# Kernel optimization log

Hardware: AMD Instinct MI355X
Metric: run time of the kernel (lower is better)

Reference implementation:

```python
import jax, jax.numpy as jnp
import numpy as np

B, L, D = 2, 1024, 1024
H, KV, CH = 16, 4, 8          # attn heads, kv heads, context-manager heads
HD = D // H                   # 64
E, K, FF = 8, 2, 4 * D        # experts, top-k, ffn hidden
DC = 4                        # conv kernel size
EPS = 1e-6


def setup_inputs() -> dict:
    key = jax.random.key(0)
    ks = jax.random.split(key, 32)
    s = 0.02
    n = lambda k, shp: jax.random.normal(k, shp, jnp.float32) * s
    return {
        'x': jax.random.normal(ks[0], (B, L, D), jnp.float32),
        'mask': jnp.ones((B, L), jnp.int32),
        'w_rms1': jnp.ones((D,), jnp.float32),
        'w_rms2': jnp.ones((D,), jnp.float32),
        'w_rms3': jnp.ones((D,), jnp.float32),
        'w_rms4': jnp.ones((D,), jnp.float32),
        'Wq': n(ks[1], (D, D)), 'Wk': n(ks[2], (D, KV * HD)),
        'Wv': n(ks[3], (D, KV * HD)), 'Wo': n(ks[4], (D, D)),
        'Cq': n(ks[5], (D, D)), 'Ck': n(ks[6], (D, D)),
        'Cv': n(ks[7], (D, D)), 'Co': n(ks[8], (D, D)),
        'Wi': n(ks[9], (D, 2 * D)), 'bi': jnp.zeros((2 * D,), jnp.float32),
        'conv_w': n(ks[10], (D, 1, DC)), 'conv_b': jnp.zeros((D,), jnp.float32),
        'Wod': n(ks[11], (D, D)), 'bod': jnp.zeros((D,), jnp.float32),
        'w_gate': n(ks[12], (E, D)),
        'W1': n(ks[13], (E, D, FF)), 'b1': jnp.zeros((E, FF), jnp.float32),
        'W2': n(ks[14], (E, FF, D)), 'b2': jnp.zeros((E, D), jnp.float32),
    }


def _rmsnorm(x, w):
    rms = jnp.sqrt(jnp.mean(x * x, axis=-1, keepdims=True) + EPS)
    return w * (x / rms)


def _mha(x, mask, Wq, Wk, Wv, Wo, nh, nkv):
    b, l, d = x.shape
    hd = d // nh
    q = (x @ Wq).reshape(b, l, nh, hd)
    k = (x @ Wk).reshape(b, l, nkv, hd)
    v = (x @ Wv).reshape(b, l, nkv, hd)
    if nh != nkv:
        rep = nh // nkv
        k = jnp.repeat(k, rep, axis=2)
        v = jnp.repeat(v, rep, axis=2)
    scores = jnp.einsum('bqhd,bkhd->bhqk', q, k) * (hd ** -0.5)
    scores = jnp.where(mask[:, None, None, :] == 0, -jnp.inf, scores)
    attn = jax.nn.softmax(scores, axis=-1)
    out = jnp.einsum('bhqk,bkhd->bqhd', attn, v).reshape(b, l, d)
    return out @ Wo


def _deltanet(x, Wi, bi, conv_w, conv_b, Wod, bod):
    gv = x @ Wi + bi
    gate, value = jnp.split(gv, 2, axis=-1)
    # depthwise causal conv1d (kernel DC, left pad DC-1, truncated to L)
    v_ncl = jnp.transpose(value, (0, 2, 1))  # [B, D, L]
    conv = jax.lax.conv_general_dilated(
        v_ncl, conv_w, window_strides=(1,), padding=[(DC - 1, 0)],
        feature_group_count=D, dimension_numbers=('NCH', 'OIH', 'NCH'))
    conv = conv + conv_b[None, :, None]
    conv = jnp.transpose(conv, (0, 2, 1))  # [B, L, D]
    gated = conv * jax.nn.silu(gate)
    return gated @ Wod + bod


def _moe(x, w_gate, W1, b1, W2, b2):
    b, l, d = x.shape
    flat = x.reshape(-1, d)                                  # [T, D]
    gate = jax.nn.softmax(flat @ w_gate.T, axis=-1)          # [T, E]
    topk_scores, topk_idx = jax.lax.top_k(gate, K)           # [T, K]
    onehot = jax.nn.one_hot(topk_idx, E, dtype=flat.dtype)   # [T, K, E]
    combine = jnp.sum(topk_scores[..., None] * onehot, axis=1)  # [T, E]
    h = jnp.einsum('td,edh->teh', flat, W1) + b1
    h = jax.nn.gelu(h, approximate=False)
    y = jnp.einsum('teh,ehd->ted', h, W2) + b2
    out = jnp.einsum('ted,te->td', y, combine)
    return out.reshape(b, l, d)


def reference(x, mask, w_rms1, w_rms2, w_rms3, w_rms4,
              Wq, Wk, Wv, Wo, Cq, Ck, Cv, Co,
              Wi, bi, conv_w, conv_b, Wod, bod,
              w_gate, W1, b1, W2, b2):
    # eval mode: dropout = identity. multi_token_pred output is discarded by the block.
    res1 = x
    h = _rmsnorm(x, w_rms1)
    h = res1 + _mha(h, mask, Wq, Wk, Wv, Wo, H, KV)
    res2 = h
    # ContextManager stand-in: 8-head softmax self-attention (source unavailable)
    cm = _mha(h, mask, Cq, Ck, Cv, Co, CH, CH)
    h = res2 + cm
    res3 = h
    g = _rmsnorm(h, w_rms2)
    h = res3 + _deltanet(g, Wi, bi, conv_w, conv_b, Wod, bod)
    res4 = h
    g = _rmsnorm(h, w_rms3)
    h = res4 + _moe(g, w_gate, W1, b1, W2, b2)
    h = _rmsnorm(h, w_rms4)
    return h
```

## Files before the change

### kernel.cpp

```cpp
#include <hip/hip_runtime.h>
#include <hip/hip_bf16.h>
#include <math.h>

#define T_TOK 2048
#define B_SZ 2
#define L_SEQ 1024
#define D_MOD 1024
#define N_H 16
#define N_KV 4
#define N_CH 8
#define N_E 8
#define FF_DIM 4096
#define DC_K 4
#define EPS_F 1e-6f

typedef unsigned short u16;
typedef unsigned int u32;
typedef short s16x8 __attribute__((ext_vector_type(8)));
typedef u16 u16x8 __attribute__((ext_vector_type(8)));
typedef float f32x4 __attribute__((ext_vector_type(4)));
struct alignas(8) U16x4 { u16 a, b, c, d; };

__device__ __forceinline__ float gelu_exact(float x) {
    return 0.5f * x * (1.0f + erff(x * 0.70710678118654752f));
}
__device__ __forceinline__ u16 f2bf(float f) {
    u32 x = __float_as_uint(f);
    return (u16)((x + 0x7fffu + ((x >> 16) & 1u)) >> 16);
}
__device__ __forceinline__ float b2f(u16 u) {
    return __uint_as_float(((u32)u) << 16);
}
__device__ __forceinline__ void gload_lds16(const u16* g, u16* l) {
    __builtin_amdgcn_global_load_lds(
        (const __attribute__((address_space(1))) u32*)g,
        (__attribute__((address_space(3))) u32*)l, 16, 0, 0);
}
__device__ __forceinline__ int swz(int row, int ch, int cpr) {
    return (cpr == 4) ? (ch ^ ((row >> 1) & 3)) : (ch ^ (row & 7));
}

struct TDesc {
    const float* src;
    u16* dst;
    int R, C, dstStride, dstRowOff, tileBase, nPerMat;
};
struct TPack { TDesc d[10]; };

__global__ __launch_bounds__(256) void transpose_all(TPack p) {
    __shared__ float ts[64][65];
    int t = blockIdx.x;
    int i = 0;
#pragma unroll
    for (int j = 1; j < 10; ++j)
        if (t >= p.d[j].tileBase) i = j;
    TDesc d = p.d[i];
    int local = t - d.tileBase;
    int e = local / d.nPerMat;
    local -= e * d.nPerMat;
    int ntx = d.C >> 6;
    int bx = local % ntx, by = local / ntx;
    const float* src = d.src + (size_t)e * d.R * d.C + (size_t)(by * 64) * d.C + bx * 64;
    u16* dst = d.dst + (size_t)e * d.C * d.dstStride +
               (size_t)(d.dstRowOff + bx * 64) * d.dstStride + by * 64;
    int tid = threadIdx.x;
#pragma unroll
    for (int k = 0; k < 4; ++k) {
        int fidx = k * 256 + tid;
        int r = fidx >> 4, c4 = (fidx & 15) << 2;
        float4 v = *(const float4*)(src + (size_t)r * d.C + c4);
        ts[r][c4] = v.x; ts[r][c4 + 1] = v.y; ts[r][c4 + 2] = v.z; ts[r][c4 + 3] = v.w;
    }
    __syncthreads();
#pragma unroll
    for (int k = 0; k < 2; ++k) {
        int idx = k * 256 + tid;
        int c = idx >> 3, r8 = (idx & 7) << 3;
        u16x8 o;
#pragma unroll
        for (int j = 0; j < 8; ++j) o[j] = f2bf(ts[r8 + j][c]);
        *(u16x8*)(dst + (size_t)c * d.dstStride + r8) = o;
    }
}

__global__ __launch_bounds__(256) void rmsnorm_kernel(const float* __restrict__ x,
                                                      const float* __restrict__ w,
                                                      float* __restrict__ fo,
                                                      u16* __restrict__ bo) {
    int row = blockIdx.x;
    int tid = threadIdx.x;
    const float* xr = x + (size_t)row * D_MOD;
    float4 v = ((const float4*)xr)[tid];
    float ss = v.x * v.x + v.y * v.y + v.z * v.z + v.w * v.w;
    __shared__ float red[256];
    red[tid] = ss;
    __syncthreads();
    for (int s = 128; s > 0; s >>= 1) {
        if (tid < s) red[tid] += red[tid + s];
        __syncthreads();
    }
    float inv = 1.0f / sqrtf(red[0] * (1.0f / D_MOD) + EPS_F);
    float4 wv = ((const float4*)w)[tid];
    float4 o;
    o.x = v.x * inv * wv.x;
    o.y = v.y * inv * wv.y;
    o.z = v.z * inv * wv.z;
    o.w = v.w * inv * wv.w;
    if (fo) ((float4*)(fo + (size_t)row * D_MOD))[tid] = o;
    if (bo) {
        U16x4 b;
        b.a = f2bf(o.x); b.b = f2bf(o.y); b.c = f2bf(o.z); b.d = f2bf(o.w);
        *(U16x4*)(bo + (size_t)row * D_MOD + tid * 4) = b;
    }
}

template <int MODE, int GELU, int OUTF, int OUTB, int BM, int BK, int TW>
__global__ __launch_bounds__(256) void mfma_gemm(const u16* __restrict__ A,
                                                 const u16* __restrict__ BT,
                                                 const float* __restrict__ bias,
                                                 const float* __restrict__ res,
                                                 float* __restrict__ C,
                                                 u16* __restrict__ Cb,
                                                 const int* __restrict__ list,
                                                 const int* __restrict__ offs,
                                                 const int* __restrict__ counts,
                                                 int M, int N, int K, int nx,
                                                 const float* __restrict__ tW1,
                                                 const float* __restrict__ tW2,
                                                 u16* __restrict__ tW1T,
                                                 u16* __restrict__ tW2T,
                                                 int tLo, int tHi) {
    constexpr int PWR = BM / 2;
    constexpr int MI = PWR / 16;
    constexpr int NI = 4;
    constexpr int CPR = BK / 8;
    constexpr int AISS = (BM * CPR) / 64;
    constexpr int BISS = (128 * CPR) / 64;
    constexpr int APW = (AISS >= 4) ? (AISS / 4) : 1;
    constexpr int BPW = BISS / 4;
    constexpr int SMG = (2 * BM * BK + 2 * 128 * BK) * 2;
    constexpr int SMT = TW ? (64 * 65 * 4) : 0;
    constexpr int SM = SMG > SMT ? SMG : SMT;
    __shared__ alignas(16) char smem[SM];
    u16* ldsA = (u16*)smem;
    u16* ldsB = ldsA + 2 * BM * BK;
    int tid = threadIdx.x;
    int lane = tid & 63, w = tid >> 6;
    int wr = w >> 1, wc = w & 1;
    int bx, by, e, sk = 0;
    if (MODE == 0) {
        bx = blockIdx.x; by = blockIdx.y; e = 0;
    } else if (MODE == 3) {
        int id = blockIdx.x;
        e = id & 7;
        int r = id >> 3;
        sk = r & 1;
        int q = r >> 1;
        bx = q % nx;
        by = q / nx;
    } else {
        int id = blockIdx.x;
        e = id & 7;
        int r = id >> 3;
        bx = r % nx;
        by = r / nx;
    }
    int cnt, off;
    if (MODE == 0) { cnt = M; off = 0; }
    else { cnt = counts[e]; off = offs[e]; }
    int m0 = by * BM;
    if (m0 < cnt) {
        int n0 = bx * 128;
        const u16* Bt = BT + (size_t)e * (size_t)N * K;
        int kLo = 0, kHi = K;
        if (MODE == 3) { kLo = sk * (K >> 1); kHi = kLo + (K >> 1); }

        const u16* aSrc[APW];
        const u16* bSrc[BPW];
#pragma unroll
        for (int jp = 0; jp < APW; ++jp) {
            int ii = (AISS >= 4) ? (jp * 4 + w) : w;
            int ci = ii * 64 + lane;
            int rowA = ci / CPR, ch = ci % CPR;
            int rl = m0 + ((rowA < BM) ? rowA : (BM - 1));
            if (rl >= cnt) rl = cnt - 1;
            size_t ga;
            if (MODE == 1) ga = (size_t)list[off + rl] * K;
            else if (MODE >= 2) ga = (size_t)(off + rl) * K;
            else ga = (size_t)rl * K;
            aSrc[jp] = A + ga + (swz(rowA, ch, CPR) << 3);
        }
#pragma unroll
        for (int jp = 0; jp < BPW; ++jp) {
            int ii = jp * 4 + w;
            int ci = ii * 64 + lane;
            int rowB = ci / CPR, ch = ci % CPR;
            bSrc[jp] = Bt + (size_t)(n0 + rowB) * K + (swz(rowB, ch, CPR) << 3);
        }

        auto stage = [&](int buf, int k0) {
#pragma unroll
            for (int jp = 0; jp < APW; ++jp) {
                if (AISS >= 4 || w < AISS) {
                    int ii = (AISS >= 4) ? (jp * 4 + w) : w;
                    gload_lds16(aSrc[jp] + k0, ldsA + buf * (BM * BK) + ii * 512);
                }
            }
#pragma unroll
            for (int jp = 0; jp < BPW; ++jp) {
                int ii = jp * 4 + w;
                gload_lds16(bSrc[jp] + k0, ldsB + buf * (128 * BK) + ii * 512);
            }
        };

        f32x4 acc[MI][NI] = {};
        int r16 = lane & 15, cr = lane >> 4;

        stage(0, kLo);
        __syncthreads();
        int cur = 0;
        for (int k0 = kLo; k0 < kHi; k0 += BK) {
            if (k0 + BK < kHi) stage(cur ^ 1, k0 + BK);
#pragma unroll
            for (int hh = 0; hh < BK / 32; ++hh) {
                s16x8 af[MI], bfr[NI];
#pragma unroll
                for (int mi = 0; mi < MI; ++mi) {
                    int row = wr * PWR + mi * 16 + r16;
                    af[mi] = *(const s16x8*)&ldsA[cur * (BM * BK) + row * BK +
                                                  (swz(row, hh * 4 + cr, CPR) << 3)];
                }
#pragma unroll
                for (int ni = 0; ni < NI; ++ni) {
                    int row = wc * 64 + ni * 16 + r16;
                    bfr[ni] = *(const s16x8*)&ldsB[cur * (128 * BK) + row * BK +
                                                   (swz(row, hh * 4 + cr, CPR) << 3)];
                }
#pragma unroll
                for (int mi = 0; mi < MI; ++mi)
#pragma unroll
                    for (int ni = 0; ni < NI; ++ni)
                        acc[mi][ni] = __builtin_amdgcn_mfma_f32_16x16x32_bf16(
                            af[mi], bfr[ni], acc[mi][ni], 0, 0, 0);
            }
            __syncthreads();
            cur ^= 1;
        }

        const float* bias_e = bias ? (bias + ((MODE && MODE != 3) ? (size_t)e * N : 0)) : nullptr;
        float* Cp = C ? (C + (MODE == 3 ? (size_t)sk * ((size_t)2 * T_TOK * 1024) : (size_t)0))
                      : nullptr;
#pragma unroll
        for (int mi = 0; mi < MI; ++mi) {
#pragma unroll
            for (int ni = 0; ni < NI; ++ni) {
                int rloc = wr * PWR + mi * 16 + (lane >> 4) * 4;
                int col = n0 + wc * 64 + ni * 16 + (lane & 15);
#pragma unroll
                for (int jj = 0; jj < 4; ++jj) {
                    int rl = m0 + rloc + jj;
                    if (rl >= cnt) continue;
                    float val = acc[mi][ni][jj];
                    if (bias_e) val += bias_e[col];
                    if (GELU) val = gelu_exact(val);
                    size_t crow = (MODE == 0) ? (size_t)rl : (size_t)(off + rl);
                    if (res) val += res[crow * N + col];
                    if (OUTF) Cp[crow * N + col] = val;
                    if (OUTB) Cb[crow * N + col] = f2bf(val);
                }
            }
        }
    }

    if constexpr (TW) {
        int nb = gridDim.x * gridDim.y;
        int bid = blockIdx.y * gridDim.x + blockIdx.x;
        float (*ts)[65] = (float(*)[65])smem;
        __syncthreads();
        for (int t = tLo + bid; t < tHi; t += nb) {
            const float* src;
            u16* dst;
            int Cc, ds;
            if (t < 8192) {
                int ee = t >> 10, loc = t & 1023;
                int tbx = loc & 63, tby = loc >> 6;
                src = tW1 + (size_t)ee * 1024 * FF_DIM + (size_t)(tby << 6) * FF_DIM + (tbx << 6);
                dst = tW1T + (size_t)ee * FF_DIM * 1024 + (size_t)(tbx << 6) * 1024 + (tby << 6);
                Cc = FF_DIM; ds = 1024;
            } else {
                int tt = t - 8192;
                int ee = tt >> 10, loc = tt & 1023;
                int tbx = loc & 15, tby = loc >> 4;
                src = tW2 + (size_t)ee * FF_DIM * 1024 + (size_t)(tby << 6) * 1024 + (tbx << 6);
                dst = tW2T + (size_t)ee * 1024 * FF_DIM + (size_t)(tbx << 6) * FF_DIM + (tby << 6);
                Cc = 1024; ds = FF_DIM;
            }
#pragma unroll
            for (int k = 0; k < 4; ++k) {
                int fidx = k * 256 + tid;
                int r = fidx >> 4, c4 = (fidx & 15) << 2;
                float4 v = *(const float4*)(src + (size_t)r * Cc + c4);
                ts[r][c4] = v.x; ts[r][c4 + 1] = v.y; ts[r][c4 + 2] = v.z; ts[r][c4 + 3] = v.w;
            }
            __syncthreads();
#pragma unroll
            for (int k = 0; k < 2; ++k) {
                int idx = k * 256 + tid;
                int c = idx >> 3, r8 = (idx & 7) << 3;
                u16x8 o;
#pragma unroll
                for (int j = 0; j < 8; ++j) o[j] = f2bf(ts[r8 + j][c]);
                *(u16x8*)(dst + (size_t)c * ds + r8) = o;
            }
            __syncthreads();
        }
    }
}

template <int HD>
__global__ __launch_bounds__(256) void mfma_attn(const u16* __restrict__ Qb,
                                                 const u16* __restrict__ Kb,
                                                 const u16* __restrict__ Vb,
                                                 u16* __restrict__ O,
                                                 int stride, int ostride,
                                                 int nh, int nkv, float scale) {
    constexpr int KT = 64;
    constexpr int CH = HD / 8;
    constexpr int NF = HD / 32;
    constexpr int ND = HD / 16;
    constexpr int VSTR = 72;
    constexpr int NISS = (64 * CH) / (64 * 4);

    __shared__ u16 Kl[64 * HD];
    __shared__ u16 Vt[HD * VSTR];
    __shared__ u16 Pl[4][16 * 72];

    int tid = threadIdx.x, lane = tid & 63, w = tid >> 6;
    int g = lane >> 4, r16 = lane & 15;
    int q0 = blockIdx.x * 64, h = blockIdx.y, b = blockIdx.z;
    int kvh = h / (nh / nkv);

    const u16* Qp = Qb + (size_t)(b * L_SEQ + q0 + w * 16 + r16) * stride + h * HD + g * 8;
    s16x8 qf[NF];
#pragma unroll
    for (int f = 0; f < NF; ++f) qf[f] = *(const s16x8*)(Qp + f * 32);

    const u16* Kbase = Kb + (size_t)(b * L_SEQ) * stride + (size_t)kvh * HD;
    const u16* Vbase = Vb + (size_t)(b * L_SEQ) * stride + (size_t)kvh * HD;

    int srcOffK[NISS];
#pragma unroll
    for (int i = 0; i < NISS; ++i) {
        int ci = (w * NISS + i) * 64 + lane;
        int row = ci / CH;
        int ch = ci % CH;
        srcOffK[i] = row * stride + ((ch ^ (row & 7)) << 3);
    }

    f32x4 ofr[ND] = {};
    float m_r[4], l_r[4];
#pragma unroll
    for (int r = 0; r < 4; ++r) { m_r[r] = -1e30f; l_r[r] = 0.f; }

    for (int kt = 0; kt < L_SEQ / KT; ++kt) {
        const u16* Ksrc = Kbase + (size_t)(kt * KT) * stride;
        const u16* Vsrc = Vbase + (size_t)(kt * KT) * stride;
        __syncthreads();
#pragma unroll
        for (int i = 0; i < NISS; ++i)
            gload_lds16(Ksrc + srcOffK[i], Kl + (size_t)(w * NISS + i) * 512);
#pragma unroll
        for (int half = 0; half < HD / 64; ++half) {
            int dbase = w * 16 + half * 64;
            u16x8 v0 = *(const u16x8*)(Vsrc + (size_t)lane * stride + dbase);
            u16x8 v1 = *(const u16x8*)(Vsrc + (size_t)lane * stride + dbase + 8);
#pragma unroll
            for (int j = 0; j < 8; ++j) {
                Vt[(dbase + j) * VSTR + lane] = v0[j];
                Vt[(dbase + 8 + j) * VSTR + lane] = v1[j];
            }
        }
        __syncthreads();

        f32x4 s[4];
        __builtin_amdgcn_s_setprio(1);
#pragma unroll
        for (int sub = 0; sub < 4; ++sub) {
            f32x4 acc = {};
#pragma unroll
            for (int f = 0; f < NF; ++f) {
                int row = sub * 16 + r16;
                int chunk = (f * 4 + g) ^ (row & 7);
                s16x8 kf = *(const s16x8*)&Kl[(row * CH + chunk) * 8];
                acc = __builtin_amdgcn_mfma_f32_16x16x32_bf16(qf[f], kf, acc, 0, 0, 0);
            }
            s[sub] = acc;
        }
        __builtin_amdgcn_s_setprio(0);

#pragma unroll
        for (int sub = 0; sub < 4; ++sub)
#pragma unroll
            for (int r = 0; r < 4; ++r) s[sub][r] *= scale;
#pragma unroll
        for (int r = 0; r < 4; ++r) {
            float mx = fmaxf(fmaxf(s[0][r], s[1][r]), fmaxf(s[2][r], s[3][r]));
            mx = fmaxf(mx, __shfl_xor(mx, 1));
            mx = fmaxf(mx, __shfl_xor(mx, 2));
            mx = fmaxf(mx, __shfl_xor(mx, 4));
            mx = fmaxf(mx, __shfl_xor(mx, 8));
            float mo = m_r[r];
            float mn = fmaxf(mo, mx);
            float sc = __expf(mo - mn);
            m_r[r] = mn;
            float sum = 0.f;
#pragma unroll
            for (int sub = 0; sub < 4; ++sub) {
                float e = __expf(s[sub][r] - mn);
                s[sub][r] = e;
                sum += e;
            }
            sum += __shfl_xor(sum, 1);
            sum += __shfl_xor(sum, 2);
            sum += __shfl_xor(sum, 4);
            sum += __shfl_xor(sum, 8);
            l_r[r] = l_r[r] * sc + sum;
#pragma unroll
            for (int dsub = 0; dsub < ND; ++dsub) ofr[dsub][r] *= sc;
        }

        u16* Pw = Pl[w];
#pragma unroll
        for (int sub = 0; sub < 4; ++sub)
#pragma unroll
            for (int r = 0; r < 4; ++r) {
                int q = g * 4 + r;
                int k = sub * 16 + r16;
                Pw[q * 72 + (((k >> 3) ^ (q & 7)) << 3) + (k & 7)] = f2bf(s[sub][r]);
            }
        __syncthreads();

        s16x8 pf[2];
#pragma unroll
        for (int ks = 0; ks < 2; ++ks) {
            int chunk = (ks * 4 + g) ^ (r16 & 7);
            pf[ks] = *(const s16x8*)&Pw[r16 * 72 + chunk * 8];
        }
        __builtin_amdgcn_s_setprio(1);
#pragma unroll
        for (int dsub = 0; dsub < ND; ++dsub)
#pragma unroll
            for (int ks = 0; ks < 2; ++ks) {
                s16x8 vf = *(const s16x8*)&Vt[(dsub * 16 + r16) * VSTR + ks * 32 + g * 8];
                ofr[dsub] = __builtin_amdgcn_mfma_f32_16x16x32_bf16(pf[ks], vf, ofr[dsub], 0, 0, 0);
            }
        __builtin_amdgcn_s_setprio(0);
    }

    float inv[4];
#pragma unroll
    for (int r = 0; r < 4; ++r) inv[r] = 1.0f / l_r[r];
#pragma unroll
    for (int dsub = 0; dsub < ND; ++dsub)
#pragma unroll
        for (int r = 0; r < 4; ++r) {
            int q = q0 + w * 16 + g * 4 + r;
            O[(size_t)(b * L_SEQ + q) * ostride + h * HD + dsub * 16 + r16] =
                f2bf(ofr[dsub][r] * inv[r]);
        }
}

__global__ __launch_bounds__(256) void conv_gate_kernel(const u16* __restrict__ gv,
                                                        const float* __restrict__ cw,
                                                        const float* __restrict__ cb,
                                                        u16* __restrict__ gated) {
    int idx = blockIdx.x * 256 + threadIdx.x;
    if (idx >= T_TOK * D_MOD / 8) return;
    int d8 = (idx & 127) << 3;
    int t = idx >> 7;
    int l = t & (L_SEQ - 1);
    float conv[8];
#pragma unroll
    for (int j = 0; j < 8; ++j) conv[j] = cb[d8 + j];
#pragma unroll
    for (int i = 0; i < DC_K; ++i) {
        int lp = l - (DC_K - 1) + i;
        if (lp >= 0) {
            u16x8 v8 = *(const u16x8*)(gv + (size_t)(t - l + lp) * (2 * D_MOD) + D_MOD + d8);
#pragma unroll
            for (int j = 0; j < 8; ++j) conv[j] += b2f(v8[j]) * cw[(d8 + j) * DC_K + i];
        }
    }
    u16x8 g8 = *(const u16x8*)(gv + (size_t)t * (2 * D_MOD) + d8);
    u16x8 o;
#pragma unroll
    for (int j = 0; j < 8; ++j) {
        float gate = b2f(g8[j]);
        float sig = 1.0f / (1.0f + expf(-gate));
        o[j] = f2bf(conv[j] * (gate * sig));
    }
    *(u16x8*)(gated + (size_t)t * D_MOD + d8) = o;
}

__global__ __launch_bounds__(256) void route_kernel(const float* __restrict__ g,
                                                    const float* __restrict__ wg,
                                                    int* __restrict__ tIdx,
                                                    float* __restrict__ tScore,
                                                    int* __restrict__ counts) {
    int t = blockIdx.x, tid = threadIdx.x;
    __shared__ float gs[D_MOD];
    __shared__ float logits[N_E];
    ((float4*)gs)[tid] = ((const float4*)(g + (size_t)t * D_MOD))[tid];
    __syncthreads();
    int e = tid >> 5, lane = tid & 31;
    const float* w = wg + (size_t)e * D_MOD;
    float p = 0.f;
    for (int d = lane; d < D_MOD; d += 32) p += gs[d] * w[d];
    for (int o = 16; o > 0; o >>= 1) p += __shfl_down(p, o, 32);
    if (lane == 0) logits[e] = p;
    __syncthreads();
    if (tid == 0) {
        float mx = logits[0];
        for (int e2 = 1; e2 < N_E; ++e2) mx = fmaxf(mx, logits[e2]);
        float pe[N_E];
        float Z = 0.f;
        for (int e2 = 0; e2 < N_E; ++e2) {
            pe[e2] = expf(logits[e2] - mx);
            Z += pe[e2];
        }
        int i0 = 0;
        float b0 = pe[0];
        for (int e2 = 1; e2 < N_E; ++e2)
            if (pe[e2] > b0) { b0 = pe[e2]; i0 = e2; }
        int i1 = -1;
        float b1 = -1.f;
        for (int e2 = 0; e2 < N_E; ++e2)
            if (e2 != i0 && pe[e2] > b1) { b1 = pe[e2]; i1 = e2; }
        float invZ = 1.0f / Z;
        tIdx[t * 2] = i0;
        tIdx[t * 2 + 1] = i1;
        tScore[t * 2] = b0 * invZ;
        tScore[t * 2 + 1] = b1 * invZ;
        atomicAdd(&counts[i0], 1);
        atomicAdd(&counts[i1], 1);
    }
}

__global__ void prefix_kernel(const int* __restrict__ counts, int* __restrict__ offs,
                              int* __restrict__ cursor) {
    if (threadIdx.x == 0) {
        int acc = 0;
        for (int e = 0; e < N_E; ++e) {
            offs[e] = acc;
            acc += counts[e];
            cursor[e] = 0;
        }
    }
}

__global__ __launch_bounds__(256) void fill_kernel(const int* __restrict__ tIdx,
                                                   const int* __restrict__ offs,
                                                   int* __restrict__ cursor,
                                                   int* __restrict__ list,
                                                   int* __restrict__ pairRow) {
    int t = blockIdx.x * 256 + threadIdx.x;
    if (t >= T_TOK) return;
    for (int kk = 0; kk < 2; ++kk) {
        int e = tIdx[t * 2 + kk];
        int pos = atomicAdd(&cursor[e], 1);
        int slot = offs[e] + pos;
        list[slot] = t;
        pairRow[t * 2 + kk] = slot;
    }
}

__global__ __launch_bounds__(256) void combine_rms_kernel(const float* __restrict__ yp,
                                                          const float* __restrict__ b2,
                                                          const float* __restrict__ tScore,
                                                          const int* __restrict__ pairRow,
                                                          const int* __restrict__ tIdx,
                                                          const float* __restrict__ h,
                                                          const float* __restrict__ w,
                                                          float* __restrict__ out) {
    const size_t HALF = (size_t)2 * T_TOK * D_MOD;
    int row = blockIdx.x;
    int tid = threadIdx.x;
    float4 v = ((const float4*)(h + (size_t)row * D_MOD))[tid];
#pragma unroll
    for (int kk = 0; kk < 2; ++kk) {
        int r = pairRow[row * 2 + kk];
        int e = tIdx[row * 2 + kk];
        float s = tScore[row * 2 + kk];
        float4 y0 = ((const float4*)(yp + (size_t)r * D_MOD))[tid];
        float4 y1 = ((const float4*)(yp + HALF + (size_t)r * D_MOD))[tid];
        float4 bb = ((const float4*)(b2 + (size_t)e * D_MOD))[tid];
        v.x += s * (y0.x + y1.x + bb.x);
        v.y += s * (y0.y + y1.y + bb.y);
        v.z += s * (y0.z + y1.z + bb.z);
        v.w += s * (y0.w + y1.w + bb.w);
    }
    __shared__ float red[256];
    red[tid] = v.x * v.x + v.y * v.y + v.z * v.z + v.w * v.w;
    __syncthreads();
    for (int s = 128; s > 0; s >>= 1) {
        if (tid < s) red[tid] += red[tid + s];
        __syncthreads();
    }
    float inv = 1.0f / sqrtf(red[0] * (1.0f / D_MOD) + EPS_F);
    float4 wv = ((const float4*)w)[tid];
    float4 o;
    o.x = v.x * inv * wv.x;
    o.y = v.y * inv * wv.y;
    o.z = v.z * inv * wv.z;
    o.w = v.w * inv * wv.w;
    ((float4*)(out + (size_t)row * D_MOD))[tid] = o;
}

extern "C" void kernel_launch(void* const* d_in, const int* in_sizes, int n_in,
                              void* d_out, int out_size, void* d_ws, size_t ws_size,
                              hipStream_t stream) {
    const float* x = (const float*)d_in[0];
    const float* w_rms1 = (const float*)d_in[2];
    const float* w_rms2 = (const float*)d_in[3];
    const float* w_rms3 = (const float*)d_in[4];
    const float* w_rms4 = (const float*)d_in[5];
    const float* Wq = (const float*)d_in[6];
    const float* Wk = (const float*)d_in[7];
    const float* Wv = (const float*)d_in[8];
    const float* Wo = (const float*)d_in[9];
    const float* Cq = (const float*)d_in[10];
    const float* Ck = (const float*)d_in[11];
    const float* Cv = (const float*)d_in[12];
    const float* Co = (const float*)d_in[13];
    const float* Wi = (const float*)d_in[14];
    const float* bi = (const float*)d_in[15];
    const float* conv_w = (const float*)d_in[16];
    const float* conv_b = (const float*)d_in[17];
    const float* Wod = (const float*)d_in[18];
    const float* bod = (const float*)d_in[19];
    const float* w_gate = (const float*)d_in[20];
    const float* W1 = (const float*)d_in[21];
    const float* b1 = (const float*)d_in[22];
    const float* W2 = (const float*)d_in[23];
    const float* b2 = (const float*)d_in[24];
    float* out = (float*)d_out;

    char* ws = (char*)d_ws;
    size_t off = 0;
    auto alloc_f = [&](size_t n) { float* p = (float*)(ws + off); off += n * 4; return p; };
    auto alloc_b = [&](size_t n) { u16* p = (u16*)(ws + off); off += n * 2; return p; };

    u16* qkvT = alloc_b((size_t)1536 * 1024);
    u16* cqkvT = alloc_b((size_t)3072 * 1024);
    u16* WoT = alloc_b((size_t)1024 * 1024);
    u16* CoT = alloc_b((size_t)1024 * 1024);
    u16* WiT = alloc_b((size_t)2048 * 1024);
    u16* WodT = alloc_b((size_t)1024 * 1024);
    u16* W1T = alloc_b((size_t)N_E * FF_DIM * 1024);
    u16* W2T = alloc_b((size_t)N_E * 1024 * FF_DIM);
    const size_t TD = (size_t)T_TOK * D_MOD;
    float* h = alloc_f(TD);
    float* nrm = alloc_f(TD);
    u16* nrm_bf = alloc_b(TD);
    u16* h_bf = alloc_b(TD);
    u16* ab_bf = alloc_b(TD);
    u16* qkv_bf = alloc_b((size_t)T_TOK * 3072);
    u16* gv_bf = alloc_b((size_t)T_TOK * 2048);
    u16* hsel = alloc_b((size_t)2 * T_TOK * FF_DIM);
    float* ypart = alloc_f((size_t)2 * 2 * T_TOK * D_MOD);
    int* counts = (int*)(ws + off); off += N_E * 4;
    int* offs = (int*)(ws + off); off += N_E * 4;
    int* cursor = (int*)(ws + off); off += N_E * 4;
    int* tIdx = (int*)(ws + off); off += 2 * T_TOK * 4;
    int* list = (int*)(ws + off); off += 2 * T_TOK * 4;
    int* pairRow = (int*)(ws + off); off += 2 * T_TOK * 4;
    float* tScore = alloc_f(2 * T_TOK);

    TPack tp;
    int tb = 0;
    auto mkd = [&](int i, const float* s, u16* d, int R, int C, int ds, int ro) {
        int per = (C >> 6) * (R >> 6);
        tp.d[i] = TDesc{s, d, R, C, ds, ro, tb, per};
        tb += per;
    };
    mkd(0, Wq, qkvT, 1024, 1024, 1024, 0);
    mkd(1, Wk, qkvT, 1024, 256, 1024, 1024);
    mkd(2, Wv, qkvT, 1024, 256, 1024, 1280);
    mkd(3, Cq, cqkvT, 1024, 1024, 1024, 0);
    mkd(4, Ck, cqkvT, 1024, 1024, 1024, 1024);
    mkd(5, Cv, cqkvT, 1024, 1024, 1024, 2048);
    mkd(6, Wo, WoT, 1024, 1024, 1024, 0);
    mkd(7, Co, CoT, 1024, 1024, 1024, 0);
    mkd(8, Wi, WiT, 1024, 2048, 1024, 0);
    mkd(9, Wod, WodT, 1024, 1024, 1024, 0);
    transpose_all<<<tb, 256, 0, stream>>>(tp);

    rmsnorm_kernel<<<T_TOK, 256, 0, stream>>>(x, w_rms1, nullptr, nrm_bf);
    mfma_gemm<0, 0, 0, 1, 32, 64, 1><<<dim3(12, 64, 1), 256, 0, stream>>>(
        nrm_bf, qkvT, nullptr, nullptr, nullptr, qkv_bf, nullptr, nullptr, nullptr,
        T_TOK, 1536, 1024, 0, W1, W2, W1T, W2T, 0, 2600);
    mfma_attn<64><<<dim3(16, N_H, B_SZ), 256, 0, stream>>>(
        qkv_bf, qkv_bf + 1024, qkv_bf + 1280, ab_bf, 1536, 1024, N_H, N_KV, 0.125f);
    mfma_gemm<0, 0, 1, 1, 32, 64, 1><<<dim3(8, 64, 1), 256, 0, stream>>>(
        ab_bf, WoT, nullptr, x, h, h_bf, nullptr, nullptr, nullptr,
        T_TOK, 1024, 1024, 0, W1, W2, W1T, W2T, 2600, 4300);

    mfma_gemm<0, 0, 0, 1, 32, 64, 1><<<dim3(24, 64, 1), 256, 0, stream>>>(
        h_bf, cqkvT, nullptr, nullptr, nullptr, qkv_bf, nullptr, nullptr, nullptr,
        T_TOK, 3072, 1024, 0, W1, W2, W1T, W2T, 4300, 9500);
    mfma_attn<128><<<dim3(16, N_CH, B_SZ), 256, 0, stream>>>(
        qkv_bf, qkv_bf + 1024, qkv_bf + 2048, ab_bf, 3072, 1024, N_CH, N_CH,
        0.088388347648318447f);
    mfma_gemm<0, 0, 1, 0, 32, 64, 1><<<dim3(8, 64, 1), 256, 0, stream>>>(
        ab_bf, CoT, nullptr, h, h, nullptr, nullptr, nullptr, nullptr,
        T_TOK, 1024, 1024, 0, W1, W2, W1T, W2T, 9500, 11200);

    rmsnorm_kernel<<<T_TOK, 256, 0, stream>>>(h, w_rms2, nullptr, nrm_bf);
    mfma_gemm<0, 0, 0, 1, 32, 64, 1><<<dim3(16, 64, 1), 256, 0, stream>>>(
        nrm_bf, WiT, bi, nullptr, nullptr, gv_bf, nullptr, nullptr, nullptr,
        T_TOK, 2048, 1024, 0, W1, W2, W1T, W2T, 11200, 14684);
    conv_gate_kernel<<<(T_TOK * D_MOD / 8 + 255) / 256, 256, 0, stream>>>(gv_bf, conv_w, conv_b, ab_bf);
    mfma_gemm<0, 0, 1, 0, 32, 64, 1><<<dim3(8, 64, 1), 256, 0, stream>>>(
        ab_bf, WodT, bod, h, h, nullptr, nullptr, nullptr, nullptr,
        T_TOK, 1024, 1024, 0, W1, W2, W1T, W2T, 14684, 16384);

    rmsnorm_kernel<<<T_TOK, 256, 0, stream>>>(h, w_rms3, nrm, nrm_bf);
    hipMemsetAsync(counts, 0, N_E * sizeof(int), stream);
    route_kernel<<<T_TOK, 256, 0, stream>>>(nrm, w_gate, tIdx, tScore, counts);
    prefix_kernel<<<1, 64, 0, stream>>>(counts, offs, cursor);
    fill_kernel<<<(T_TOK + 255) / 256, 256, 0, stream>>>(tIdx, offs, cursor, list, pairRow);
    mfma_gemm<1, 1, 0, 1, 128, 32, 0><<<32 * 16 * 8, 256, 0, stream>>>(
        nrm_bf, W1T, b1, nullptr, nullptr, hsel, list, offs, counts,
        T_TOK, FF_DIM, 1024, 32, nullptr, nullptr, nullptr, nullptr, 0, 0);
    mfma_gemm<3, 0, 1, 0, 64, 32, 0><<<2 * 8 * 32 * 8, 256, 0, stream>>>(
        hsel, W2T, nullptr, nullptr, ypart, nullptr, list, offs, counts,
        T_TOK, 1024, FF_DIM, 8, nullptr, nullptr, nullptr, nullptr, 0, 0);
    combine_rms_kernel<<<T_TOK, 256, 0, stream>>>(ypart, b2, tScore, pairRow, tIdx, h,
                                                  w_rms4, out);
}
```

Measured before the change: 586.7 us.

## Double-buffer K/V tiles in attention and widen MoE up-projection GEMM tile

The attention kernel now double-buffers the K and V LDS tiles. It prefetches the next K tile with async global-to-LDS loads and the next V tile into registers while the current tile is computed, and it replaces one barrier with an lgkmcnt wait plus barrier. The GEMM template gains a BN parameter, and the MoE W1 GEMM uses a 128x256 tile with half as many column blocks, so each A tile is reused across more output columns. The cost is more LDS and register pressure, which may reduce occupancy in attention and the expert GEMM.

```diff
diff --git a/kernel.cpp b/kernel.cpp
--- a/kernel.cpp
+++ b/kernel.cpp
@@ -20,6 +20,8 @@
 typedef u16 u16x8 __attribute__((ext_vector_type(8)));
 typedef float f32x4 __attribute__((ext_vector_type(4)));
 struct alignas(8) U16x4 { u16 a, b, c, d; };
+
+#define BAR_LGKM() asm volatile("s_waitcnt lgkmcnt(0)\n\ts_barrier" ::: "memory")
 
 __device__ __forceinline__ float gelu_exact(float x) {
     return 0.5f * x * (1.0f + erff(x * 0.70710678118654752f));
@@ -114,7 +116,7 @@
     }
 }
 
-template <int MODE, int GELU, int OUTF, int OUTB, int BM, int BK, int TW>
+template <int MODE, int GELU, int OUTF, int OUTB, int BM, int BN, int BK, int TW>
 __global__ __launch_bounds__(256) void mfma_gemm(const u16* __restrict__ A,
                                                  const u16* __restrict__ BT,
                                                  const float* __restrict__ bias,
@@ -131,14 +133,15 @@
                                                  u16* __restrict__ tW2T,
                                                  int tLo, int tHi) {
     constexpr int PWR = BM / 2;
+    constexpr int PWC = BN / 2;
     constexpr int MI = PWR / 16;
-    constexpr int NI = 4;
+    constexpr int NI = PWC / 16;
     constexpr int CPR = BK / 8;
     constexpr int AISS = (BM * CPR) / 64;
-    constexpr int BISS = (128 * CPR) / 64;
+    constexpr int BISS = (BN * CPR) / 64;
     constexpr int APW = (AISS >= 4) ? (AISS / 4) : 1;
     constexpr int BPW = BISS / 4;
-    constexpr int SMG = (2 * BM * BK + 2 * 128 * BK) * 2;
+    constexpr int SMG = (2 * BM * BK + 2 * BN * BK) * 2;
     constexpr int SMT = TW ? (64 * 65 * 4) : 0;
     constexpr int SM = SMG > SMT ? SMG : SMT;
     __shared__ alignas(16) char smem[SM];
@@ -170,7 +173,7 @@
     else { cnt = counts[e]; off = offs[e]; }
     int m0 = by * BM;
     if (m0 < cnt) {
-        int n0 = bx * 128;
+        int n0 = bx * BN;
         const u16* Bt = BT + (size_t)e * (size_t)N * K;
         int kLo = 0, kHi = K;
         if (MODE == 3) { kLo = sk * (K >> 1); kHi = kLo + (K >> 1); }
@@ -209,7 +212,7 @@
 #pragma unroll
             for (int jp = 0; jp < BPW; ++jp) {
                 int ii = jp * 4 + w;
-                gload_lds16(bSrc[jp] + k0, ldsB + buf * (128 * BK) + ii * 512);
+                gload_lds16(bSrc[jp] + k0, ldsB + buf * (BN * BK) + ii * 512);
             }
         };
 
@@ -232,8 +235,8 @@
                 }
 #pragma unroll
                 for (int ni = 0; ni < NI; ++ni) {
-                    int row = wc * 64 + ni * 16 + r16;
-                    bfr[ni] = *(const s16x8*)&ldsB[cur * (128 * BK) + row * BK +
+                    int row = wc * PWC + ni * 16 + r16;
+                    bfr[ni] = *(const s16x8*)&ldsB[cur * (BN * BK) + row * BK +
                                                    (swz(row, hh * 4 + cr, CPR) << 3)];
                 }
 #pragma unroll
@@ -255,7 +258,7 @@
 #pragma unroll
             for (int ni = 0; ni < NI; ++ni) {
                 int rloc = wr * PWR + mi * 16 + (lane >> 4) * 4;
-                int col = n0 + wc * 64 + ni * 16 + (lane & 15);
+                int col = n0 + wc * PWC + ni * 16 + (lane & 15);
 #pragma unroll
                 for (int jj = 0; jj < 4; ++jj) {
                     int rl = m0 + rloc + jj;
@@ -330,9 +333,10 @@
     constexpr int ND = HD / 16;
     constexpr int VSTR = 72;
     constexpr int NISS = (64 * CH) / (64 * 4);
-
-    __shared__ u16 Kl[64 * HD];
-    __shared__ u16 Vt[HD * VSTR];
+    constexpr int NH2 = HD / 64;
+
+    __shared__ u16 Kl[2][64 * HD];
+    __shared__ u16 Vt[2][HD * VSTR];
     __shared__ u16 Pl[4][16 * 72];
 
     int tid = threadIdx.x, lane = tid & 63, w = tid >> 6;
@@ -357,30 +361,47 @@
         srcOffK[i] = row * stride + ((ch ^ (row & 7)) << 3);
     }
 
+    u16x8 vr[2 * NH2];
+    auto vload = [&](int kt) {
+        const u16* Vs = Vbase + (size_t)(kt * KT) * stride + (size_t)lane * stride;
+#pragma unroll
+        for (int half = 0; half < NH2; ++half) {
+            int dbase = w * 16 + half * 64;
+            vr[2 * half] = *(const u16x8*)(Vs + dbase);
+            vr[2 * half + 1] = *(const u16x8*)(Vs + dbase + 8);
+        }
+    };
+
     f32x4 ofr[ND] = {};
     float m_r[4], l_r[4];
 #pragma unroll
     for (int r = 0; r < 4; ++r) { m_r[r] = -1e30f; l_r[r] = 0.f; }
 
-    for (int kt = 0; kt < L_SEQ / KT; ++kt) {
-        const u16* Ksrc = Kbase + (size_t)(kt * KT) * stride;
-        const u16* Vsrc = Vbase + (size_t)(kt * KT) * stride;
+    constexpr int NT = L_SEQ / KT;
+#pragma unroll
+    for (int i = 0; i < NISS; ++i)
+        gload_lds16(Kbase + srcOffK[i], &Kl[0][(w * NISS + i) * 512]);
+    vload(0);
+
+    for (int kt = 0; kt < NT; ++kt) {
+        int cur = kt & 1;
+#pragma unroll
+        for (int half = 0; half < NH2; ++half) {
+            int dbase = w * 16 + half * 64;
+#pragma unroll
+            for (int j = 0; j < 8; ++j) {
+                Vt[cur][(dbase + j) * VSTR + lane] = vr[2 * half][j];
+                Vt[cur][(dbase + 8 + j) * VSTR + lane] = vr[2 * half + 1][j];
+            }
+        }
         __syncthreads();
-#pragma unroll
-        for (int i = 0; i < NISS; ++i)
-            gload_lds16(Ksrc + srcOffK[i], Kl + (size_t)(w * NISS + i) * 512);
-#pragma unroll
-        for (int half = 0; half < HD / 64; ++half) {
-            int dbase = w * 16 + half * 64;
-            u16x8 v0 = *(const u16x8*)(Vsrc + (size_t)lane * stride + dbase);
-            u16x8 v1 = *(const u16x8*)(Vsrc + (size_t)lane * stride + dbase + 8);
-#pragma unroll
-            for (int j = 0; j < 8; ++j) {
-                Vt[(dbase + j) * VSTR + lane] = v0[j];
-                Vt[(dbase + 8 + j) * VSTR + lane] = v1[j];
-            }
-        }
-        __syncthreads();
+        if (kt + 1 < NT) {
+            const u16* Ksrc2 = Kbase + (size_t)((kt + 1) * KT) * stride;
+#pragma unroll
+            for (int i = 0; i < NISS; ++i)
+                gload_lds16(Ksrc2 + srcOffK[i], &Kl[cur ^ 1][(w * NISS + i) * 512]);
+            vload(kt + 1);
+        }
 
         f32x4 s[4];
         __builtin_amdgcn_s_setprio(1);
@@ -391,7 +412,7 @@
             for (int f = 0; f < NF; ++f) {
                 int row = sub * 16 + r16;
                 int chunk = (f * 4 + g) ^ (row & 7);
-                s16x8 kf = *(const s16x8*)&Kl[(row * CH + chunk) * 8];
+                s16x8 kf = *(const s16x8*)&Kl[cur][(row * CH + chunk) * 8];
                 acc = __builtin_amdgcn_mfma_f32_16x16x32_bf16(qf[f], kf, acc, 0, 0, 0);
             }
             s[sub] = acc;
@@ -438,7 +459,7 @@
                 int k = sub * 16 + r16;
                 Pw[q * 72 + (((k >> 3) ^ (q & 7)) << 3) + (k & 7)] = f2bf(s[sub][r]);
             }
-        __syncthreads();
+        BAR_LGKM();
 
         s16x8 pf[2];
 #pragma unroll
@@ -451,7 +472,7 @@
         for (int dsub = 0; dsub < ND; ++dsub)
 #pragma unroll
             for (int ks = 0; ks < 2; ++ks) {
-                s16x8 vf = *(const s16x8*)&Vt[(dsub * 16 + r16) * VSTR + ks * 32 + g * 8];
+                s16x8 vf = *(const s16x8*)&Vt[cur][(dsub * 16 + r16) * VSTR + ks * 32 + g * 8];
                 ofr[dsub] = __builtin_amdgcn_mfma_f32_16x16x32_bf16(pf[ks], vf, ofr[dsub], 0, 0, 0);
             }
         __builtin_amdgcn_s_setprio(0);
@@ -696,31 +717,31 @@
     transpose_all<<<tb, 256, 0, stream>>>(tp);
 
     rmsnorm_kernel<<<T_TOK, 256, 0, stream>>>(x, w_rms1, nullptr, nrm_bf);
-    mfma_gemm<0, 0, 0, 1, 32, 64, 1><<<dim3(12, 64, 1), 256, 0, stream>>>(
+    mfma_gemm<0, 0, 0, 1, 32, 128, 64, 1><<<dim3(12, 64, 1), 256, 0, stream>>>(
         nrm_bf, qkvT, nullptr, nullptr, nullptr, qkv_bf, nullptr, nullptr, nullptr,
         T_TOK, 1536, 1024, 0, W1, W2, W1T, W2T, 0, 2600);
     mfma_attn<64><<<dim3(16, N_H, B_SZ), 256, 0, stream>>>(
         qkv_bf, qkv_bf + 1024, qkv_bf + 1280, ab_bf, 1536, 1024, N_H, N_KV, 0.125f);
-    mfma_gemm<0, 0, 1, 1, 32, 64, 1><<<dim3(8, 64, 1), 256, 0, stream>>>(
+    mfma_gemm<0, 0, 1, 1, 32, 128, 64, 1><<<dim3(8, 64, 1), 256, 0, stream>>>(
         ab_bf, WoT, nullptr, x, h, h_bf, nullptr, nullptr, nullptr,
         T_TOK, 1024, 1024, 0, W1, W2, W1T, W2T, 2600, 4300);
 
-    mfma_gemm<0, 0, 0, 1, 32, 64, 1><<<dim3(24, 64, 1), 256, 0, stream>>>(
+    mfma_gemm<0, 0, 0, 1, 32, 128, 64, 1><<<dim3(24, 64, 1), 256, 0, stream>>>(
         h_bf, cqkvT, nullptr, nullptr, nullptr, qkv_bf, nullptr, nullptr, nullptr,
         T_TOK, 3072, 1024, 0, W1, W2, W1T, W2T, 4300, 9500);
     mfma_attn<128><<<dim3(16, N_CH, B_SZ), 256, 0, stream>>>(
         qkv_bf, qkv_bf + 1024, qkv_bf + 2048, ab_bf, 3072, 1024, N_CH, N_CH,
         0.088388347648318447f);
-    mfma_gemm<0, 0, 1, 0, 32, 64, 1><<<dim3(8, 64, 1), 256, 0, stream>>>(
+    mfma_gemm<0, 0, 1, 0, 32, 128, 64, 1><<<dim3(8, 64, 1), 256, 0, stream>>>(
         ab_bf, CoT, nullptr, h, h, nullptr, nullptr, nullptr, nullptr,
         T_TOK, 1024, 1024, 0, W1, W2, W1T, W2T, 9500, 11200);
 
     rmsnorm_kernel<<<T_TOK, 256, 0, stream>>>(h, w_rms2, nullptr, nrm_bf);
-    mfma_gemm<0, 0, 0, 1, 32, 64, 1><<<dim3(16, 64, 1), 256, 0, stream>>>(
+    mfma_gemm<0, 0, 0, 1, 32, 128, 64, 1><<<dim3(16, 64, 1), 256, 0, stream>>>(
         nrm_bf, WiT, bi, nullptr, nullptr, gv_bf, nullptr, nullptr, nullptr,
         T_TOK, 2048, 1024, 0, W1, W2, W1T, W2T, 11200, 14684);
     conv_gate_kernel<<<(T_TOK * D_MOD / 8 + 255) / 256, 256, 0, stream>>>(gv_bf, conv_w, conv_b, ab_bf);
-    mfma_gemm<0, 0, 1, 0, 32, 64, 1><<<dim3(8, 64, 1), 256, 0, stream>>>(
+    mfma_gemm<0, 0, 1, 0, 32, 128, 64, 1><<<dim3(8, 64, 1), 256, 0, stream>>>(
         ab_bf, WodT, bod, h, h, nullptr, nullptr, nullptr, nullptr,
         T_TOK, 1024, 1024, 0, W1, W2, W1T, W2T, 14684, 16384);
 
@@ -729,10 +750,10 @@
     route_kernel<<<T_TOK, 256, 0, stream>>>(nrm, w_gate, tIdx, tScore, counts);
     prefix_kernel<<<1, 64, 0, stream>>>(counts, offs, cursor);
     fill_kernel<<<(T_TOK + 255) / 256, 256, 0, stream>>>(tIdx, offs, cursor, list, pairRow);
-    mfma_gemm<1, 1, 0, 1, 128, 32, 0><<<32 * 16 * 8, 256, 0, stream>>>(
+    mfma_gemm<1, 1, 0, 1, 128, 256, 32, 0><<<16 * 16 * 8, 256, 0, stream>>>(
         nrm_bf, W1T, b1, nullptr, nullptr, hsel, list, offs, counts,
-        T_TOK, FF_DIM, 1024, 32, nullptr, nullptr, nullptr, nullptr, 0, 0);
-    mfma_gemm<3, 0, 1, 0, 64, 32, 0><<<2 * 8 * 32 * 8, 256, 0, stream>>>(
+        T_TOK, FF_DIM, 1024, 16, nullptr, nullptr, nullptr, nullptr, 0, 0);
+    mfma_gemm<3, 0, 1, 0, 64, 128, 32, 0><<<2 * 8 * 32 * 8, 256, 0, stream>>>(
         hsel, W2T, nullptr, nullptr, ypart, nullptr, list, offs, counts,
         T_TOK, 1024, FF_DIM, 8, nullptr, nullptr, nullptr, nullptr, 0, 0);
     combine_rms_kernel<<<T_TOK, 256, 0, stream>>>(ypart, b2, tScore, pairRow, tIdx, h,
```

Measured after the change: 679.5 us. +15.8%, slower.
